# Kernel optimization log

Measured on AMD Instinct MI355X. Metric: run time of the kernel, lower is better.

## Reference

```python
import jax, jax.numpy as jnp
import numpy as np

POOL_SIZE = 7
NUM_ROIS = 1000
H, W, C = 128, 128, 1024


def setup_inputs() -> dict:
    key = jax.random.key(0)
    k_img, k_xy, k_wh = jax.random.split(key, 3)
    img = jax.random.normal(k_img, (1, H, W, C), dtype=jnp.float32)
    # rois[0, i] = (x, y, w, h) in feature-map pixel units; ensure x+w<=W, y+h<=H
    xy = jax.random.randint(k_xy, (1, NUM_ROIS, 2), 0, 64, dtype=jnp.int32)
    wh = jax.random.randint(k_wh, (1, NUM_ROIS, 2), 8, 65, dtype=jnp.int32)
    rois = jnp.concatenate([xy, wh], axis=-1)  # [1, num_rois, 4]
    return {"img": img, "rois": rois}


def _axis_coords(start, size, out_size):
    """Half-pixel-center bilinear source coords for a crop [start, start+size).

    Matches tf.image.resize(method='bilinear', antialias=False): src = (i+0.5)*scale - 0.5,
    clamped to the crop, then split into floor index / +1 index / lerp weight.
    """
    size_f = size.astype(jnp.float32)
    f = (jnp.arange(out_size, dtype=jnp.float32) + 0.5) * (size_f / out_size) - 0.5
    f = jnp.clip(f, 0.0, jnp.maximum(size_f - 1.0, 0.0))
    i0 = jnp.floor(f).astype(jnp.int32)
    i1 = jnp.minimum(i0 + 1, size - 1)
    wgt = f - i0.astype(jnp.float32)
    return start + i0, start + i1, wgt


def _pool_one_roi(img2d, roi):
    # img2d: [H, W, C]; roi: [4] int32 (x, y, w, h)
    x, y, w, h = roi[0], roi[1], roi[2], roi[3]
    y0, y1, wy = _axis_coords(y, h, POOL_SIZE)  # each [P]
    x0, x1, wx = _axis_coords(x, w, POOL_SIZE)
    v00 = img2d[y0[:, None], x0[None, :], :]  # [P, P, C]
    v01 = img2d[y0[:, None], x1[None, :], :]
    v10 = img2d[y1[:, None], x0[None, :], :]
    v11 = img2d[y1[:, None], x1[None, :], :]
    wy = wy[:, None, None]
    wx = wx[None, :, None]
    top = v00 * (1.0 - wx) + v01 * wx
    bot = v10 * (1.0 - wx) + v11 * wx
    return top * (1.0 - wy) + bot * wy


def reference(img, rois):
    # Vectorized RoiPoolingConv.call: batched crop + bilinear resize over all ROIs.
    pooled = jax.vmap(_pool_one_roi, in_axes=(None, 0))(img[0], rois[0])  # [R, P, P, C]
    return pooled[None]  # [1, num_rois, P, P, C]
```

## Files before the change

kernel.cpp:

```cpp
#include <hip/hip_runtime.h>

#define POOL 7
#define NROIS 1000
#define IMG_H 128
#define IMG_W 128
#define NCH 1024

typedef float f4 __attribute__((ext_vector_type(4)));

__global__ __launch_bounds__(256) void roi_pool_kernel(
    const float* __restrict__ img,
    const int* __restrict__ rois,
    float* __restrict__ out)
{
    const int bid  = blockIdx.x;
    const int roi  = bid / 49;
    const int cell = bid - roi * 49;
    const int py   = cell / 7;
    const int px   = cell - py * 7;

    const int4 r = ((const int4*)rois)[roi];
    const int x = r.x, y = r.y, w = r.z, h = r.w;

    const float hf = (float)h;
    float fy = ((float)py + 0.5f) * (hf / (float)POOL) - 0.5f;
    fy = fminf(fmaxf(fy, 0.0f), fmaxf(hf - 1.0f, 0.0f));
    const int   iy0 = (int)floorf(fy);
    const int   iy1 = min(iy0 + 1, h - 1);
    const float wy  = fy - (float)iy0;
    const int   y0  = y + iy0;
    const int   y1  = y + iy1;

    const float wf = (float)w;
    float fx = ((float)px + 0.5f) * (wf / (float)POOL) - 0.5f;
    fx = fminf(fmaxf(fx, 0.0f), fmaxf(wf - 1.0f, 0.0f));
    const int   ix0 = (int)floorf(fx);
    const int   ix1 = min(ix0 + 1, w - 1);
    const float wx  = fx - (float)ix0;
    const int   x0  = x + ix0;
    const int   x1  = x + ix1;

    const f4* p00 = (const f4*)(img + ((size_t)y0 * IMG_W + x0) * NCH);
    const f4* p01 = (const f4*)(img + ((size_t)y0 * IMG_W + x1) * NCH);
    const f4* p10 = (const f4*)(img + ((size_t)y1 * IMG_W + x0) * NCH);
    const f4* p11 = (const f4*)(img + ((size_t)y1 * IMG_W + x1) * NCH);
    f4* po = (f4*)(out + (size_t)bid * NCH);

    const int t = threadIdx.x;

    const f4 a = p00[t];
    const f4 b = p01[t];
    const f4 c = p10[t];
    const f4 d = p11[t];

    const float owx = 1.0f - wx;
    const float owy = 1.0f - wy;

    const f4 top = a * owx + b * wx;
    const f4 bot = c * owx + d * wx;
    const f4 res = top * owy + bot * wy;

    __builtin_nontemporal_store(res, po + t);
}

extern "C" void kernel_launch(void* const* d_in, const int* in_sizes, int n_in,
                              void* d_out, int out_size, void* d_ws, size_t ws_size,
                              hipStream_t stream)
{
    const float* img  = (const float*)d_in[0];
    const int*   rois = (const int*)d_in[1];
    float*       out  = (float*)d_out;

    const int nblocks = NROIS * POOL * POOL;
    roi_pool_kernel<<<nblocks, 256, 0, stream>>>(img, rois, out);
}
```

Measured before the change: 316.4 us.

## Partition channels into groups mapped per XCD for L2 locality of image gathers

Remaps the grid so each block handles 32 ROI cells for a 32-channel slice, with channel groups assigned to XCDs via blockIdx low bits and processed in phases. This is meant to shrink each XCD's working set of gathered image data so bilinear neighbor reads hit in L2 instead of going to the infinity cache or HBM. In exchange, each cell's output write becomes a 128-byte fragment strided across rows, which may reduce write coalescing.

```diff
diff --git a/kernel.cpp b/kernel.cpp
--- a/kernel.cpp
+++ b/kernel.cpp
@@ -2,9 +2,16 @@
 
 #define POOL 7
 #define NROIS 1000
-#define IMG_H 128
+#define NCELLS (NROIS * POOL * POOL)
 #define IMG_W 128
 #define NCH 1024
+
+#define CG 32
+#define NG (NCH / CG)
+#define CELLS_PER_BLK 32
+#define BLKS_PER_GROUP ((NCELLS + CELLS_PER_BLK - 1) / CELLS_PER_BLK)
+#define NXCD 8
+#define PHASES (NG / NXCD)
 
 typedef float f4 __attribute__((ext_vector_type(4)));
 
@@ -13,11 +20,21 @@
     const int* __restrict__ rois,
     float* __restrict__ out)
 {
-    const int bid  = blockIdx.x;
-    const int roi  = bid / 49;
-    const int cell = bid - roi * 49;
-    const int py   = cell / 7;
-    const int px   = cell - py * 7;
+    const unsigned bid   = blockIdx.x;
+    const unsigned xcd   = bid & 7u;
+    const unsigned slot  = bid >> 3;
+    const unsigned phase = slot / BLKS_PER_GROUP;
+    const unsigned cblk  = slot - phase * BLKS_PER_GROUP;
+    const unsigned g     = phase * NXCD + xcd;
+
+    const unsigned t    = threadIdx.x;
+    const unsigned cell = cblk * CELLS_PER_BLK + (t >> 3);
+    if (cell >= NCELLS) return;
+
+    const unsigned roi = cell / 49u;
+    const unsigned c49 = cell - roi * 49u;
+    const unsigned py  = c49 / 7u;
+    const unsigned px  = c49 - py * 7u;
 
     const int4 r = ((const int4*)rois)[roi];
     const int x = r.x, y = r.y, w = r.z, h = r.w;
@@ -40,18 +57,18 @@
     const int   x0  = x + ix0;
     const int   x1  = x + ix1;
 
-    const f4* p00 = (const f4*)(img + ((size_t)y0 * IMG_W + x0) * NCH);
-    const f4* p01 = (const f4*)(img + ((size_t)y0 * IMG_W + x1) * NCH);
-    const f4* p10 = (const f4*)(img + ((size_t)y1 * IMG_W + x0) * NCH);
-    const f4* p11 = (const f4*)(img + ((size_t)y1 * IMG_W + x1) * NCH);
-    f4* po = (f4*)(out + (size_t)bid * NCH);
+    const unsigned choff = g * CG + (t & 7u) * 4u;
 
-    const int t = threadIdx.x;
+    const f4* p00 = (const f4*)(img + ((size_t)y0 * IMG_W + x0) * NCH + choff);
+    const f4* p01 = (const f4*)(img + ((size_t)y0 * IMG_W + x1) * NCH + choff);
+    const f4* p10 = (const f4*)(img + ((size_t)y1 * IMG_W + x0) * NCH + choff);
+    const f4* p11 = (const f4*)(img + ((size_t)y1 * IMG_W + x1) * NCH + choff);
+    f4* po = (f4*)(out + (size_t)cell * NCH + choff);
 
-    const f4 a = p00[t];
-    const f4 b = p01[t];
-    const f4 c = p10[t];
-    const f4 d = p11[t];
+    const f4 a = *p00;
+    const f4 b = *p01;
+    const f4 c = *p10;
+    const f4 d = *p11;
 
     const float owx = 1.0f - wx;
     const float owy = 1.0f - wy;
@@ -60,7 +77,7 @@
     const f4 bot = c * owx + d * wx;
     const f4 res = top * owy + bot * wy;
 
-    __builtin_nontemporal_store(res, po + t);
+    __builtin_nontemporal_store(res, po);
 }
 
 extern "C" void kernel_launch(void* const* d_in, const int* in_sizes, int n_in,
@@ -71,6 +88,6 @@
     const int*   rois = (const int*)d_in[1];
     float*       out  = (float*)d_out;
 
-    const int nblocks = NROIS * POOL * POOL;
+    const int nblocks = BLKS_PER_GROUP * NG;
     roi_pool_kernel<<<nblocks, 256, 0, stream>>>(img, rois, out);
 }
```

New measurement: 302.2 us. 4.5% less time.
